# Performance work log

Hardware: AMD Instinct MI355X
Metric: run time of the kernel (lower is better)

## Reference

```python
import jax, jax.numpy as jnp
import numpy as np
from math import comb

H, W = 256, 256          # canvas_shape
NUM_SAMPLES = 32         # bezier samples per curve
K = 4                    # control points per curve (cubic bezier)
WIDTH = 4.0
AAF = 0.35               # anti_aliasing_factor
EPSILON = 1e-6


def _bernstein_basis(num_samples: int, k: int) -> jnp.ndarray:
    """[S, K] Bernstein basis evaluated at uniform ts in [0, 1]."""
    ts = jnp.linspace(0.0, 1.0, num_samples, dtype=jnp.float32)  # get_uniform_ts
    i = jnp.arange(k, dtype=jnp.float32)
    binom = jnp.array([comb(k - 1, j) for j in range(k)], dtype=jnp.float32)
    return binom * ts[:, None] ** i * (1.0 - ts[:, None]) ** (k - 1 - i)


def setup_inputs() -> dict:
    key = jax.random.key(0)
    # normalized key points in [0, 1], shape [B, K, 2]
    inputs = jax.random.uniform(key, (32, K, 2), dtype=jnp.float32)
    return {"inputs": inputs}


def reference(inputs):
    B = inputs.shape[0]
    canvas_shape = jnp.array([H, W], dtype=jnp.float32)
    key_points = inputs * canvas_shape                      # [B, K, 2] in pixel coords

    basis = _bernstein_basis(NUM_SAMPLES, K)                # [S, K]
    samples = jnp.einsum('sk,bkd->bsd', basis, key_points)  # [B, S, 2]

    # pixel grid, p = [y, x] as in the torch loop
    ys, xs = jnp.meshgrid(jnp.arange(H, dtype=jnp.float32),
                          jnp.arange(W, dtype=jnp.float32), indexing='ij')
    pts = jnp.stack([ys, xs], axis=-1).reshape(-1, 2)       # [N, 2], N = H*W

    # squared distances via ||p||^2 - 2 p.s + ||s||^2 (GEMM form)
    p2 = jnp.sum(pts * pts, axis=-1)                        # [N]
    s2 = jnp.sum(samples * samples, axis=-1)                # [B, S]
    cross = jnp.einsum('nd,bsd->bns', pts, samples)         # [B, N, S]
    d2 = p2[None, :, None] - 2.0 * cross + s2[:, None, :]   # [B, N, S]

    min_d = jnp.sqrt(jnp.maximum(jnp.min(d2, axis=-1), 0.0))  # [B, N]
    canvas = 1.0 - (min_d / WIDTH + EPSILON) ** AAF
    return canvas.reshape(B, H, W)
```

## Files before the change

kernel.cpp:

```cpp
#include <hip/hip_runtime.h>
#include <math.h>

#define OPAQ(x) asm volatile("" : "+v"(x))

#define HH 256
#define WW 256
#define NS 32
#define NB 32

__device__ __forceinline__ float rlane(float v, int lane) {
    int i = __builtin_amdgcn_readlane(__builtin_bit_cast(int, v), lane);
    return __builtin_bit_cast(float, i);
}
__device__ __forceinline__ float hw_sqrt(float x) {
    float r; asm("v_sqrt_f32 %0, %1" : "=v"(r) : "v"(x)); return r;
}
__device__ __forceinline__ float hw_log2(float x) {
    float r; asm("v_log_f32 %0, %1" : "=v"(r) : "v"(x)); return r;
}
__device__ __forceinline__ float hw_exp2(float x) {
    float r; asm("v_exp_f32 %0, %1" : "=v"(r) : "v"(x)); return r;
}

__device__ __forceinline__ void curve_sample(const float* kp, int s,
                                             float& accy_o, float& accx_o, float& s2_o) {
    const float STEP = 1.0f / 31.0f;
    float t = (float)s * STEP; OPAQ(t);
    float u = 1.0f - t;        OPAQ(u);
    float t2 = (float)((double)t * (double)t);
    float t3 = (float)((double)t * (double)t * (double)t);
    float u2 = (float)((double)u * (double)u);
    float u3 = (float)((double)u * (double)u * (double)u);
    float b0 = u3;
    float m1 = 3.0f * t;  OPAQ(m1); float b1 = m1 * u2; OPAQ(b1);
    float m2 = 3.0f * t2; OPAQ(m2); float b2 = m2 * u;  OPAQ(b2);
    float b3 = t3;

    float ky0 = kp[0] * 256.0f, kx0 = kp[1] * 256.0f;
    float ky1 = kp[2] * 256.0f, kx1 = kp[3] * 256.0f;
    float ky2 = kp[4] * 256.0f, kx2 = kp[5] * 256.0f;
    float ky3 = kp[6] * 256.0f, kx3 = kp[7] * 256.0f;

    float p, accy, accx;
    p = b0 * ky0; OPAQ(p); accy = p;
    p = b1 * ky1; OPAQ(p); accy = accy + p; OPAQ(accy);
    p = b2 * ky2; OPAQ(p); accy = accy + p; OPAQ(accy);
    p = b3 * ky3; OPAQ(p); accy = accy + p; OPAQ(accy);

    p = b0 * kx0; OPAQ(p); accx = p;
    p = b1 * kx1; OPAQ(p); accx = accx + p; OPAQ(accx);
    p = b2 * kx2; OPAQ(p); accx = accx + p; OPAQ(accx);
    p = b3 * kx3; OPAQ(p); accx = accx + p; OPAQ(accx);

    float q1 = accy * accy; OPAQ(q1);
    float q2 = accx * accx; OPAQ(q2);
    accy_o = accy; accx_o = accx; s2_o = q1 + q2;
}

__global__ __launch_bounds__(256) void curve_render_kernel(
    const float* __restrict__ in, float* __restrict__ out)
{
    const int b    = blockIdx.x >> 6;
    const int rg   = blockIdx.x & 63;
    const int wid  = threadIdx.x >> 6;
    const int lane = threadIdx.x & 63;
    const int row  = (rg << 2) + wid;

    float v_sy, v_sx, v_s2;
    curve_sample(in + b * 8, lane & 31, v_sy, v_sx, v_s2);

    const float y  = (float)row;
    const float x0 = (float)(lane << 2);
    const float x1 = x0 + 1.0f, x2 = x0 + 2.0f, x3 = x0 + 3.0f;
    const float p20 = y * y + x0 * x0;
    const float p21 = y * y + x1 * x1;
    const float p22 = y * y + x2 * x2;
    const float p23 = y * y + x3 * x3;

    const float INF = 3.4028234663852886e38f;
    float m0 = INF, m1 = INF, m2 = INF, m3 = INF;

    #pragma unroll
    for (int s = 0; s < NS; ++s) {
        const float sy_s = rlane(v_sy, s);
        const float sx_s = rlane(v_sx, s);
        const float s2_s = rlane(v_s2, s);
        float c0 = y * sy_s; OPAQ(c0);
        float c, e, d2;
        c = fmaf(x0, sx_s, c0); e = p20 - 2.0f * c; d2 = e + s2_s; m0 = fminf(m0, d2);
        c = fmaf(x1, sx_s, c0); e = p21 - 2.0f * c; d2 = e + s2_s; m1 = fminf(m1, d2);
        c = fmaf(x2, sx_s, c0); e = p22 - 2.0f * c; d2 = e + s2_s; m2 = fminf(m2, d2);
        c = fmaf(x3, sx_s, c0); e = p23 - 2.0f * c; d2 = e + s2_s; m3 = fminf(m3, d2);
    }

    float o0, o1, o2, o3;
    {
        float md = hw_sqrt(fmaxf(m0, 0.0f));
        float r  = fmaf(md, 0.25f, 1e-6f);
        o0 = 1.0f - hw_exp2(0.35f * hw_log2(r));
    }
    {
        float md = hw_sqrt(fmaxf(m1, 0.0f));
        float r  = fmaf(md, 0.25f, 1e-6f);
        o1 = 1.0f - hw_exp2(0.35f * hw_log2(r));
    }
    {
        float md = hw_sqrt(fmaxf(m2, 0.0f));
        float r  = fmaf(md, 0.25f, 1e-6f);
        o2 = 1.0f - hw_exp2(0.35f * hw_log2(r));
    }
    {
        float md = hw_sqrt(fmaxf(m3, 0.0f));
        float r  = fmaf(md, 0.25f, 1e-6f);
        o3 = 1.0f - hw_exp2(0.35f * hw_log2(r));
    }

    const int idx = (b * HH + row) * WW + (lane << 2);
    *reinterpret_cast<float4*>(out + idx) = make_float4(o0, o1, o2, o3);
}

extern "C" void kernel_launch(void* const* d_in, const int* in_sizes, int n_in,
                              void* d_out, int out_size, void* d_ws, size_t ws_size,
                              hipStream_t stream) {
    const float* in = (const float*)d_in[0];
    float* out = (float*)d_out;
    curve_render_kernel<<<dim3(NB * 64), dim3(256), 0, stream>>>(in, out);
}
```

Measured before the change: 16.24 us.

## Use packed FP32 math and eight pixels per thread with half the blocks

The distance inner loop now uses v_pk_mul/v_pk_fma/v_pk_add so each instruction handles two pixels, with each sample value read once per loop step and duplicated into a 64-bit scalar pair. Each thread now covers eight pixels instead of four: a wave spans two rows with 32 lanes per row, and the grid is halved. The goal is to cut VALU instruction count and spread the per-sample readlane cost over more pixels. In exchange there are fewer waves to hide latency, more registers per thread, and two float4 stores per thread.

```diff
diff --git a/kernel.cpp b/kernel.cpp
--- a/kernel.cpp
+++ b/kernel.cpp
@@ -2,15 +2,28 @@
 #include <math.h>
 
 #define OPAQ(x) asm volatile("" : "+v"(x))
+typedef float f2 __attribute__((ext_vector_type(2)));
 
 #define HH 256
 #define WW 256
 #define NS 32
 #define NB 32
 
-__device__ __forceinline__ float rlane(float v, int lane) {
-    int i = __builtin_amdgcn_readlane(__builtin_bit_cast(int, v), lane);
-    return __builtin_bit_cast(float, i);
+__device__ __forceinline__ uint64_t rlane_dup(float v, int lane) {
+    unsigned u = (unsigned)__builtin_amdgcn_readlane(__builtin_bit_cast(int, v), lane);
+    return ((uint64_t)u << 32) | (uint64_t)u;
+}
+__device__ __forceinline__ f2 pk_mul_vs(f2 a, uint64_t b) {
+    f2 d; asm("v_pk_mul_f32 %0, %1, %2" : "=v"(d) : "v"(a), "s"(b)); return d;
+}
+__device__ __forceinline__ f2 pk_fma_vsv(f2 a, uint64_t b, f2 c) {
+    f2 d; asm("v_pk_fma_f32 %0, %1, %2, %3" : "=v"(d) : "v"(a), "s"(b), "v"(c)); return d;
+}
+__device__ __forceinline__ f2 pk_fma_vvv(f2 a, f2 b, f2 c) {
+    f2 d; asm("v_pk_fma_f32 %0, %1, %2, %3" : "=v"(d) : "v"(a), "v"(b), "v"(c)); return d;
+}
+__device__ __forceinline__ f2 pk_add_vs(f2 a, uint64_t b) {
+    f2 d; asm("v_pk_add_f32 %0, %1, %2" : "=v"(d) : "v"(a), "s"(b)); return d;
 }
 __device__ __forceinline__ float hw_sqrt(float x) {
     float r; asm("v_sqrt_f32 %0, %1" : "=v"(r) : "v"(x)); return r;
@@ -60,63 +73,63 @@
 __global__ __launch_bounds__(256) void curve_render_kernel(
     const float* __restrict__ in, float* __restrict__ out)
 {
-    const int b    = blockIdx.x >> 6;
-    const int rg   = blockIdx.x & 63;
+    const int b    = blockIdx.x >> 5;
+    const int rg   = blockIdx.x & 31;
     const int wid  = threadIdx.x >> 6;
     const int lane = threadIdx.x & 63;
-    const int row  = (rg << 2) + wid;
+    const int row  = (rg << 3) + (wid << 1) + (lane >> 5);
+    const int xb   = (lane & 31) << 3;
 
     float v_sy, v_sx, v_s2;
     curve_sample(in + b * 8, lane & 31, v_sy, v_sx, v_s2);
 
-    const float y  = (float)row;
-    const float x0 = (float)(lane << 2);
-    const float x1 = x0 + 1.0f, x2 = x0 + 2.0f, x3 = x0 + 3.0f;
-    const float p20 = y * y + x0 * x0;
-    const float p21 = y * y + x1 * x1;
-    const float p22 = y * y + x2 * x2;
-    const float p23 = y * y + x3 * x3;
+    const float y = (float)row;
+    f2 yp = {y, y};
+    const f2 M2 = {-2.0f, -2.0f};
+
+    f2 xp0 = {(float)xb,       (float)(xb + 1)};
+    f2 xp1 = {(float)(xb + 2), (float)(xb + 3)};
+    f2 xp2 = {(float)(xb + 4), (float)(xb + 5)};
+    f2 xp3 = {(float)(xb + 6), (float)(xb + 7)};
+    const float yy = y * y;
+    f2 q0 = {yy + xp0.x * xp0.x, yy + xp0.y * xp0.y};
+    f2 q1 = {yy + xp1.x * xp1.x, yy + xp1.y * xp1.y};
+    f2 q2 = {yy + xp2.x * xp2.x, yy + xp2.y * xp2.y};
+    f2 q3 = {yy + xp3.x * xp3.x, yy + xp3.y * xp3.y};
 
     const float INF = 3.4028234663852886e38f;
     float m0 = INF, m1 = INF, m2 = INF, m3 = INF;
+    float m4 = INF, m5 = INF, m6 = INF, m7 = INF;
 
     #pragma unroll
     for (int s = 0; s < NS; ++s) {
-        const float sy_s = rlane(v_sy, s);
-        const float sx_s = rlane(v_sx, s);
-        const float s2_s = rlane(v_s2, s);
-        float c0 = y * sy_s; OPAQ(c0);
-        float c, e, d2;
-        c = fmaf(x0, sx_s, c0); e = p20 - 2.0f * c; d2 = e + s2_s; m0 = fminf(m0, d2);
-        c = fmaf(x1, sx_s, c0); e = p21 - 2.0f * c; d2 = e + s2_s; m1 = fminf(m1, d2);
-        c = fmaf(x2, sx_s, c0); e = p22 - 2.0f * c; d2 = e + s2_s; m2 = fminf(m2, d2);
-        c = fmaf(x3, sx_s, c0); e = p23 - 2.0f * c; d2 = e + s2_s; m3 = fminf(m3, d2);
+        const uint64_t syy = rlane_dup(v_sy, s);
+        const uint64_t sxx = rlane_dup(v_sx, s);
+        const uint64_t s22 = rlane_dup(v_s2, s);
+        f2 c0 = pk_mul_vs(yp, syy);
+        f2 c, e, d;
+        c = pk_fma_vsv(xp0, sxx, c0); e = pk_fma_vvv(c, M2, q0); d = pk_add_vs(e, s22);
+        m0 = fminf(m0, d.x); m1 = fminf(m1, d.y);
+        c = pk_fma_vsv(xp1, sxx, c0); e = pk_fma_vvv(c, M2, q1); d = pk_add_vs(e, s22);
+        m2 = fminf(m2, d.x); m3 = fminf(m3, d.y);
+        c = pk_fma_vsv(xp2, sxx, c0); e = pk_fma_vvv(c, M2, q2); d = pk_add_vs(e, s22);
+        m4 = fminf(m4, d.x); m5 = fminf(m5, d.y);
+        c = pk_fma_vsv(xp3, sxx, c0); e = pk_fma_vvv(c, M2, q3); d = pk_add_vs(e, s22);
+        m6 = fminf(m6, d.x); m7 = fminf(m7, d.y);
     }
 
-    float o0, o1, o2, o3;
-    {
-        float md = hw_sqrt(fmaxf(m0, 0.0f));
-        float r  = fmaf(md, 0.25f, 1e-6f);
-        o0 = 1.0f - hw_exp2(0.35f * hw_log2(r));
-    }
-    {
-        float md = hw_sqrt(fmaxf(m1, 0.0f));
-        float r  = fmaf(md, 0.25f, 1e-6f);
-        o1 = 1.0f - hw_exp2(0.35f * hw_log2(r));
-    }
-    {
-        float md = hw_sqrt(fmaxf(m2, 0.0f));
-        float r  = fmaf(md, 0.25f, 1e-6f);
-        o2 = 1.0f - hw_exp2(0.35f * hw_log2(r));
-    }
-    {
-        float md = hw_sqrt(fmaxf(m3, 0.0f));
-        float r  = fmaf(md, 0.25f, 1e-6f);
-        o3 = 1.0f - hw_exp2(0.35f * hw_log2(r));
-    }
+    float o0, o1, o2, o3, o4, o5, o6, o7;
+    #define TAIL(mi, oi) { \
+        float md = hw_sqrt(fmaxf(mi, 0.0f)); \
+        float r  = fmaf(md, 0.25f, 1e-6f); \
+        oi = 1.0f - hw_exp2(0.35f * hw_log2(r)); }
+    TAIL(m0, o0) TAIL(m1, o1) TAIL(m2, o2) TAIL(m3, o3)
+    TAIL(m4, o4) TAIL(m5, o5) TAIL(m6, o6) TAIL(m7, o7)
+    #undef TAIL
 
-    const int idx = (b * HH + row) * WW + (lane << 2);
-    *reinterpret_cast<float4*>(out + idx) = make_float4(o0, o1, o2, o3);
+    const int idx = (b * HH + row) * WW + xb;
+    *reinterpret_cast<float4*>(out + idx)     = make_float4(o0, o1, o2, o3);
+    *reinterpret_cast<float4*>(out + idx + 4) = make_float4(o4, o5, o6, o7);
 }
 
 extern "C" void kernel_launch(void* const* d_in, const int* in_sizes, int n_in,
@@ -124,5 +137,5 @@
                               hipStream_t stream) {
     const float* in = (const float*)d_in[0];
     float* out = (float*)d_out;
-    curve_render_kernel<<<dim3(NB * 64), dim3(256), 0, stream>>>(in, out);
+    curve_render_kernel<<<dim3(NB * 32), dim3(256), 0, stream>>>(in, out);
 }
```

After: 13.14 us (median of 2 runs). -19.1%, faster.
